# Performance work log

Measured on AMD Instinct MI355X. Metric: run time of the kernel, lower is better.

## Reference

```python
import jax, jax.numpy as jnp
import numpy as np


def _iterative_pinv(mat, n_iter=6):
    # mat: [b, h, m, m]
    m = mat.shape[-1]
    I = jnp.eye(m, dtype=mat.dtype)
    # global (over all batch/heads) scaling, matching torch.max over full tensor
    init_coef = jnp.max(jnp.sum(jnp.abs(mat), axis=-2)) * jnp.max(jnp.sum(jnp.abs(mat), axis=-1))
    out = jnp.swapaxes(mat, -2, -1) / init_coef
    for _ in range(n_iter):
        mo = jnp.matmul(mat, out)          # [b,h,m,m]
        term1 = 7.0 * I - mo
        term2 = 15.0 * I - jnp.matmul(mo, term1)
        term3 = 13.0 * I - jnp.matmul(mo, term2)
        out = 0.25 * jnp.matmul(out, term3)
    return out


def _landmarks(x, m):
    # x: [b, h, s, d] -> segment means [b, h, m, d]
    b, h, s, d = x.shape
    l = s // m
    return x.reshape(b, h, m, l, d).mean(axis=-2)


def setup_inputs() -> dict:
    key = jax.random.key(0)
    kq, kk, kv = jax.random.split(key, 3)
    shape = (4, 12, 4096, 64)
    return {
        "query": jax.random.normal(kq, shape, dtype=jnp.float32),
        "key": jax.random.normal(kk, shape, dtype=jnp.float32),
        "value": jax.random.normal(kv, shape, dtype=jnp.float32),
        "num_landmarks": 64,
    }


def reference(query, key, value, num_landmarks):
    b, h, s, d = query.shape
    scale = 1.0 / jnp.sqrt(jnp.asarray(d, dtype=query.dtype))
    q_lm = _landmarks(query, num_landmarks)   # [b,h,m,d]
    k_lm = _landmarks(key, num_landmarks)     # [b,h,m,d]
    # F_tilde: [b,h,s,m]
    F_tilde = jax.nn.softmax(jnp.einsum('bhsd,bhmd->bhsm', query, k_lm) * scale, axis=-1)
    # A_tilde: pinv of [b,h,m,m]
    A_tilde = _iterative_pinv(
        jax.nn.softmax(jnp.einsum('bhnd,bhmd->bhnm', q_lm, k_lm) * scale, axis=-1))
    # B_tilde: [b,h,m,s]
    B_tilde = jax.nn.softmax(jnp.einsum('bhmd,bhsd->bhms', q_lm, key) * scale, axis=-1)
    # out = F_tilde @ (A_tilde @ (B_tilde @ value))  -> [b,h,s,d]
    bv = jnp.matmul(B_tilde, value)        # [b,h,m,d]
    abv = jnp.matmul(A_tilde, bv)          # [b,h,m,d]
    return jnp.matmul(F_tilde, abv)        # [b,h,s,d]
```

## Files before the change

### kernel.cpp

```cpp
#include <hip/hip_runtime.h>
#include <math.h>

#define BH 48
#define Ss 4096
#define Dd 64
#define Mm 64
#define NCH 16
#define SCALE 0.125f
#define PLN 4096

typedef unsigned int u32;
typedef unsigned short u16;
typedef __attribute__((ext_vector_type(8))) short short8;
typedef __attribute__((ext_vector_type(4))) float floatx4;

union FRAG { uint4 u; short8 s; };

#define MFMA(a,b,c) __builtin_amdgcn_mfma_f32_16x16x32_bf16(a,b,c,0,0,0)

__device__ __forceinline__ u32 pack2_hi(float a, float b) {
    return (__float_as_uint(a) >> 16) | (__float_as_uint(b) & 0xFFFF0000u);
}
__device__ __forceinline__ float trunc_bf(float a) {
    return __uint_as_float(__float_as_uint(a) & 0xFFFF0000u);
}
__device__ __forceinline__ void split1(float v, u16& h, u16& l) {
    u32 u = __float_as_uint(v);
    h = (u16)(u >> 16);
    float r = v - __uint_as_float(u & 0xFFFF0000u);
    l = (u16)(__float_as_uint(r) >> 16);
}
__device__ __forceinline__ void split8(const float* v, short8& h, short8& l) {
    FRAG H, L;
    float r[8];
#pragma unroll
    for (int i = 0; i < 8; i++) r[i] = v[i] - trunc_bf(v[i]);
    H.u.x = pack2_hi(v[0], v[1]); H.u.y = pack2_hi(v[2], v[3]);
    H.u.z = pack2_hi(v[4], v[5]); H.u.w = pack2_hi(v[6], v[7]);
    L.u.x = pack2_hi(r[0], r[1]); L.u.y = pack2_hi(r[2], r[3]);
    L.u.z = pack2_hi(r[4], r[5]); L.u.w = pack2_hi(r[6], r[7]);
    h = H.s; l = L.s;
}
__device__ __forceinline__ int swz(int row, int col) {
    return row * 64 + ((((col >> 3) ^ (row & 7)) << 3) | (col & 7));
}

__global__ __launch_bounds__(256) void k_landmarks(const float* __restrict__ Q,
                                                   const float* __restrict__ Kg,
                                                   float* __restrict__ qlm,
                                                   float* __restrict__ klm,
                                                   u16* __restrict__ qlmh, u16* __restrict__ qlml,
                                                   u16* __restrict__ klmh, u16* __restrict__ klml) {
    int g = blockIdx.x, bh = blockIdx.y;
    int t = threadIdx.x;
    int seg = t >> 4, d4 = t & 15;
    int m = g * 16 + seg;
    const float* src = blockIdx.z ? Kg : Q;
    float* dst = blockIdx.z ? klm : qlm;
    u16* dh = blockIdx.z ? klmh : qlmh;
    u16* dl = blockIdx.z ? klml : qlml;
    const float* base = src + ((size_t)bh * Ss + (size_t)m * 64) * Dd + d4 * 4;
    float4 acc = make_float4(0.f, 0.f, 0.f, 0.f);
#pragma unroll
    for (int l = 0; l < 64; l++) {
        float4 v = *(const float4*)(base + (size_t)l * Dd);
        acc.x += v.x; acc.y += v.y; acc.z += v.z; acc.w += v.w;
    }
    acc.x *= (1.f / 64.f); acc.y *= (1.f / 64.f);
    acc.z *= (1.f / 64.f); acc.w *= (1.f / 64.f);
    int idx = (bh * Mm + m) * Dd + d4 * 4;
    *(float4*)(dst + idx) = acc;
    float vv[4] = {acc.x, acc.y, acc.z, acc.w};
    u16 hh[4], ll[4];
#pragma unroll
    for (int i = 0; i < 4; i++) split1(vv[i], hh[i], ll[i]);
    *(uint2*)(dh + idx) = make_uint2((u32)hh[0] | ((u32)hh[1] << 16), (u32)hh[2] | ((u32)hh[3] << 16));
    *(uint2*)(dl + idx) = make_uint2((u32)ll[0] | ((u32)ll[1] << 16), (u32)ll[2] | ((u32)ll[3] << 16));
}

__global__ __launch_bounds__(256) void k_lmsm(const float* __restrict__ qlm,
                                              const float* __restrict__ klm,
                                              float* __restrict__ smat,
                                              unsigned int* __restrict__ coef) {
    int bh = blockIdx.x, t = threadIdx.x;
    __shared__ float kl[Mm * Dd];
    __shared__ float ql[Mm * Dd];
    __shared__ float Lp[Mm][Mm + 1];
    const float4* kb = (const float4*)(klm + bh * Mm * Dd);
    const float4* qb = (const float4*)(qlm + bh * Mm * Dd);
    for (int i = t; i < Mm * Dd / 4; i += 256) {
        ((float4*)kl)[i] = kb[i];
        ((float4*)ql)[i] = qb[i];
    }
    __syncthreads();
    int n = t >> 2, c = t & 3;
    float p[16];
#pragma unroll
    for (int jj = 0; jj < 16; jj++) {
        int m = c * 16 + jj;
        float s = 0.f;
#pragma unroll
        for (int d4 = 0; d4 < 16; d4++) {
            int d = (((d4 + c * 4) & 15)) * 4;
            float4 kv = *(const float4*)(kl + m * Dd + d);
            float4 qv = *(const float4*)(ql + n * Dd + d);
            s += qv.x * kv.x + qv.y * kv.y + qv.z * kv.z + qv.w * kv.w;
        }
        p[jj] = s * SCALE;
    }
    float mx = -INFINITY;
#pragma unroll
    for (int jj = 0; jj < 16; jj++) mx = fmaxf(mx, p[jj]);
    mx = fmaxf(mx, __shfl_xor(mx, 1));
    mx = fmaxf(mx, __shfl_xor(mx, 2));
    float den = 0.f;
#pragma unroll
    for (int jj = 0; jj < 16; jj++) { p[jj] = __expf(p[jj] - mx); den += p[jj]; }
    den += __shfl_xor(den, 1);
    den += __shfl_xor(den, 2);
    float inv = 1.0f / den;
#pragma unroll
    for (int jj = 0; jj < 16; jj++) Lp[n][c * 16 + jj] = p[jj] * inv;
    __syncthreads();
    float* sg = smat + bh * Mm * Mm;
    for (int i = t; i < Mm * Mm; i += 256) sg[i] = Lp[i >> 6][i & 63];
    if (t < Mm) {
        float cs = 0.f;
#pragma unroll
        for (int nn = 0; nn < Mm; nn++) cs += Lp[nn][t];
#pragma unroll
        for (int off = 1; off < 64; off <<= 1) cs = fmaxf(cs, __shfl_xor(cs, off));
        if (t == 0) atomicMax(coef + 0, __float_as_uint(cs));
    } else if (t < 2 * Mm) {
        int nn = t - Mm; float rs = 0.f;
#pragma unroll
        for (int m = 0; m < Mm; m++) rs += Lp[nn][m];
#pragma unroll
        for (int off = 1; off < 64; off <<= 1) rs = fmaxf(rs, __shfl_xor(rs, off));
        if (t == Mm) atomicMax(coef + 1, __float_as_uint(rs));
    }
}

__device__ __forceinline__ void pinv_pass(const u16* __restrict__ Ah, const u16* __restrict__ Al,
                                          const u16* __restrict__ Bph, const u16* __restrict__ Bpl,
                                          u16* __restrict__ Oh, u16* __restrict__ Ol,
                                          int w, int c, int hi,
                                          float diag, float sgn, float scl) {
    short8 bfh[2], bfl[2];
#pragma unroll
    for (int ks = 0; ks < 2; ks++) {
        bfh[ks] = *(const short8*)&Bph[swz(w * 16 + c, ks * 32 + hi * 8)];
        bfl[ks] = *(const short8*)&Bpl[swz(w * 16 + c, ks * 32 + hi * 8)];
    }
    int j = w * 16 + c;
#pragma unroll
    for (int ta = 0; ta < 4; ta++) {
        floatx4 acc = (floatx4){0.f, 0.f, 0.f, 0.f};
#pragma unroll
        for (int ks = 0; ks < 2; ks++) {
            short8 afh = *(const short8*)&Ah[swz(ta * 16 + c, ks * 32 + hi * 8)];
            short8 afl = *(const short8*)&Al[swz(ta * 16 + c, ks * 32 + hi * 8)];
            acc = MFMA(afh, bfh[ks], acc);
            acc = MFMA(afl, bfh[ks], acc);
            acc = MFMA(afh, bfl[ks], acc);
        }
        u16 oh[4], ol[4];
#pragma unroll
        for (int r = 0; r < 4; r++) {
            int i = ta * 16 + hi * 4 + r;
            float v = scl * (((i == j) ? diag : 0.f) + sgn * acc[r]);
            split1(v, oh[r], ol[r]);
        }
        int o0 = swz(j, ta * 16 + hi * 4);
        *(u32*)&Oh[o0]     = (u32)oh[0] | ((u32)oh[1] << 16);
        *(u32*)&Oh[o0 + 2] = (u32)oh[2] | ((u32)oh[3] << 16);
        *(u32*)&Ol[o0]     = (u32)ol[0] | ((u32)ol[1] << 16);
        *(u32*)&Ol[o0 + 2] = (u32)ol[2] | ((u32)ol[3] << 16);
    }
}

__global__ __launch_bounds__(256) void k_pinv(const float* __restrict__ smat,
                                              const unsigned int* __restrict__ coef,
                                              float* __restrict__ atil) {
    extern __shared__ u16 P[];
    u16* FaH  = P;             u16* FaL  = P + PLN;
    u16* FxcH = P + 2 * PLN;   u16* FxcL = P + 3 * PLN;
    u16* X0H  = P + 4 * PLN;   u16* X0L  = P + 5 * PLN;
    u16* X1H  = P + 6 * PLN;   u16* X1L  = P + 7 * PLN;
    u16* T1H  = P + 8 * PLN;   u16* T1L  = P + 9 * PLN;
    u16* T2H  = P + 10 * PLN;  u16* T2L  = P + 11 * PLN;
    int bh = blockIdx.x, t = threadIdx.x;
    int w = t >> 6, l = t & 63, c = l & 15, hi = l >> 4;
    float inv = 1.0f / (__uint_as_float(coef[0]) * __uint_as_float(coef[1]));
    {
        int r = t >> 2, kq = (t & 3) * 16;
        const float* ar = smat + bh * 4096 + r * 64 + kq;
        float v[16];
#pragma unroll
        for (int q = 0; q < 4; q++) {
            float4 x = *(const float4*)(ar + q * 4);
            v[q * 4 + 0] = x.x; v[q * 4 + 1] = x.y; v[q * 4 + 2] = x.z; v[q * 4 + 3] = x.w;
        }
        short8 h0, l0, h1, l1;
        split8(v, h0, l0); split8(v + 8, h1, l1);
        *(short8*)&FaH[swz(r, kq)] = h0;     *(short8*)&FaH[swz(r, kq + 8)] = h1;
        *(short8*)&FaL[swz(r, kq)] = l0;     *(short8*)&FaL[swz(r, kq + 8)] = l1;
        float vs[16];
#pragma unroll
        for (int q = 0; q < 16; q++) vs[q] = v[q] * inv;
        split8(vs, h0, l0); split8(vs + 8, h1, l1);
        *(short8*)&FxcH[swz(r, kq)] = h0;    *(short8*)&FxcH[swz(r, kq + 8)] = h1;
        *(short8*)&FxcL[swz(r, kq)] = l0;    *(short8*)&FxcL[swz(r, kq + 8)] = l1;
#pragma unroll
        for (int q = 0; q < 16; q++) {
            u16 h, lo; split1(vs[q], h, lo);
            X0H[swz(kq + q, r)] = h;
            X0L[swz(kq + q, r)] = lo;
        }
    }
    __syncthreads();
    u16 *xrH = X0H, *xrL = X0L, *moH = X1H, *moL = X1L;
    for (int it = 0; it < 6; it++) {
        pinv_pass(FxcH, FxcL, FaH, FaL, moH, moL, w, c, hi, 0.f, 1.f, 1.f);
        pinv_pass(FaH, FaL, FxcH, FxcL, T1H, T1L, w, c, hi, 7.f, -1.f, 1.f);
        __syncthreads();
        pinv_pass(moH, moL, T1H, T1L, T2H, T2L, w, c, hi, 15.f, -1.f, 1.f);
        __syncthreads();
        pinv_pass(moH, moL, T2H, T2L, T1H, T1L, w, c, hi, 13.f, -1.f, 1.f);
        __syncthreads();
        pinv_pass(T1H, T1L, xrH, xrL, moH, moL, w, c, hi, 0.f, 1.f, 0.25f);
        pinv_pass(xrH, xrL, T1H, T1L, FxcH, FxcL, w, c, hi, 0.f, 1.f, 0.25f);
        __syncthreads();
        u16* th = xrH; xrH = moH; moH = th;
        u16* tl = xrL; xrL = moL; moL = tl;
    }
    {
        int i = t >> 2, j0 = (t & 3) * 16;
        FRAG h0, l0, h1, l1;
        h0.s = *(const short8*)&xrH[swz(i, j0)];
        l0.s = *(const short8*)&xrL[swz(i, j0)];
        h1.s = *(const short8*)&xrH[swz(i, j0 + 8)];
        l1.s = *(const short8*)&xrL[swz(i, j0 + 8)];
        float* ob = atil + bh * 4096 + i * 64 + j0;
#pragma unroll
        for (int q = 0; q < 8; q++) {
            ob[q]     = __uint_as_float(((u32)(u16)h0.s[q]) << 16) + __uint_as_float(((u32)(u16)l0.s[q]) << 16);
            ob[q + 8] = __uint_as_float(((u32)(u16)h1.s[q]) << 16) + __uint_as_float(((u32)(u16)l1.s[q]) << 16);
        }
    }
}

__global__ __launch_bounds__(256) void k_bvp(const float* __restrict__ Kg,
                                             const float* __restrict__ Vg,
                                             const u16* __restrict__ qlmh,
                                             const u16* __restrict__ qlml,
                                             float* __restrict__ pnum,
                                             float* __restrict__ pden) {
    __shared__ __align__(16) u16 Pb[2][4096];
    __shared__ __align__(16) u16 vt[2][4096];
    __shared__ __align__(16) float tmp[64 * 68];
    int ch = blockIdx.x, bh = blockIdx.y;
    int t = threadIdx.x, w = t >> 6, l = t & 63, c = l & 15, hi = l >> 4;
    const float* Kbh = Kg + (size_t)bh * Ss * Dd;
    const float* Vbh = Vg + (size_t)bh * Ss * Dd;
    const u16* qh = qlmh + bh * Mm * Dd;
    const u16* ql = qlml + bh * Mm * Dd;
    floatx4 pvC[4];
    float denacc[16];
#pragma unroll
    for (int i = 0; i < 4; i++) pvC[i] = (floatx4){0.f, 0.f, 0.f, 0.f};
#pragma unroll
    for (int i = 0; i < 16; i++) denacc[i] = 0.f;

    for (int tile = 0; tile < 4; ++tile) {
        int s0 = ch * 256 + tile * 64;
        __syncthreads();
        {
            int sl = t >> 2, q = (t & 3) * 16;
            const float4* vp = (const float4*)(Vbh + (size_t)(s0 + sl) * Dd + q);
            float4* dp = (float4*)(tmp + sl * 68 + q);
#pragma unroll
            for (int qq = 0; qq < 4; qq++) dp[qq] = vp[qq];
        }
        {
            int srow = s0 + w * 16 + c;
            const float* kp = Kbh + (size_t)srow * Dd + hi * 8;
            short8 kbh[2], kbl[2];
#pragma unroll
            for (int ks = 0; ks < 2; ks++) {
                float kv[8];
                float4 a = *(const float4*)(kp + ks * 32);
                float4 b = *(const float4*)(kp + ks * 32 + 4);
                kv[0] = a.x; kv[1] = a.y; kv[2] = a.z; kv[3] = a.w;
                kv[4] = b.x; kv[5] = b.y; kv[6] = b.z; kv[7] = b.w;
                split8(kv, kbh[ks], kbl[ks]);
            }
            floatx4 qkC[4];
#pragma unroll
            for (int i = 0; i < 4; i++) qkC[i] = (floatx4){0.f, 0.f, 0.f, 0.f};
#pragma unroll
            for (int mt = 0; mt < 4; mt++) {
#pragma unroll
                for (int ks = 0; ks < 2; ks++) {
                    short8 aH = *(const short8*)&qh[(mt * 16 + c) * 64 + ks * 32 + hi * 8];
                    short8 aL = *(const short8*)&ql[(mt * 16 + c) * 64 + ks * 32 + hi * 8];
                    qkC[mt] = MFMA(aH, kbh[ks], qkC[mt]);
                    qkC[mt] = MFMA(aL, kbh[ks], qkC[mt]);
                    qkC[mt] = MFMA(aH, kbl[ks], qkC[mt]);
                }
            }
#pragma unroll
            for (int mt = 0; mt < 4; mt++) {
#pragma unroll
                for (int r = 0; r < 4; r++) {
                    float pv = __expf(qkC[mt][r] * SCALE);
                    denacc[mt * 4 + r] += pv;
                    int m = mt * 16 + hi * 4 + r;
                    u16 h, lo; split1(pv, h, lo);
                    Pb[0][swz(m, w * 16 + c)] = h;
                    Pb[1][swz(m, w * 16 + c)] = lo;
                }
            }
        }
        __syncthreads();
        {
            int d = t >> 2, sg = t & 3;
            float v[16];
#pragma unroll
            for (int j = 0; j < 16; j++) v[j] = tmp[(sg * 16 + j) * 68 + d];
            short8 h0, l0, h1, l1;
            split8(v, h0, l0); split8(v + 8, h1, l1);
            *(short8*)&vt[0][swz(d, sg * 16)] = h0;
            *(short8*)&vt[0][swz(d, sg * 16 + 8)] = h1;
            *(short8*)&vt[1][swz(d, sg * 16)] = l0;
            *(short8*)&vt[1][swz(d, sg * 16 + 8)] = l1;
        }
        __syncthreads();
#pragma unroll
        for (int ks = 0; ks < 2; ks++) {
            short8 pah = *(const short8*)&Pb[0][swz(w * 16 + c, ks * 32 + hi * 8)];
            short8 pal = *(const short8*)&Pb[1][swz(w * 16 + c, ks * 32 + hi * 8)];
#pragma unroll
            for (int dt = 0; dt < 4; dt++) {
                short8 vh = *(const short8*)&vt[0][swz(dt * 16 + c, ks * 32 + hi * 8)];
                short8 vl = *(const short8*)&vt[1][swz(dt * 16 + c, ks * 32 + hi * 8)];
                pvC[dt] = MFMA(pah, vh, pvC[dt]);
                pvC[dt] = MFMA(pal, vh, pvC[dt]);
                pvC[dt] = MFMA(pah, vl, pvC[dt]);
            }
        }
    }
    float* nb = pnum + (size_t)(bh * NCH + ch) * 4096;
#pragma unroll
    for (int dt = 0; dt < 4; dt++)
#pragma unroll
        for (int r = 0; r < 4; r++)
            nb[(w * 16 + hi * 4 + r) * 64 + dt * 16 + c] = pvC[dt][r];
#pragma unroll
    for (int i = 0; i < 16; i++) {
        float v = denacc[i];
        v += __shfl_xor(v, 1); v += __shfl_xor(v, 2);
        v += __shfl_xor(v, 4); v += __shfl_xor(v, 8);
        denacc[i] = v;
    }
    if (c == 0) {
        float* db = pden + (size_t)((bh * NCH + ch) * 4 + w) * 64;
#pragma unroll
        for (int mt = 0; mt < 4; mt++)
#pragma unroll
            for (int r = 0; r < 4; r++)
                db[mt * 16 + hi * 4 + r] = denacc[mt * 4 + r];
    }
}

__global__ __launch_bounds__(256) void k_bvc(const float* __restrict__ pnum,
                                             const float* __restrict__ pden,
                                             const float* __restrict__ atil,
                                             u16* __restrict__ abvh,
                                             u16* __restrict__ abvl) {
    int bh = blockIdx.x, t = threadIdx.x;
    __shared__ float bvs[Mm][Dd + 1];
    __shared__ float Ams[Mm * (Mm + 1)];
    const float* ab = atil + bh * Mm * Mm;
    for (int i = t; i < Mm * Mm; i += 256) Ams[(i >> 6) * 65 + (i & 63)] = ab[i];
    int m = t >> 2, c = t & 3, d0 = c * 16;
    float den = 0.f;
    const float* db = pden + (size_t)bh * NCH * 4 * 64;
#pragma unroll
    for (int i = 0; i < NCH * 4; i++) den += db[i * 64 + m];
    float acc[16];
#pragma unroll
    for (int i = 0; i < 16; i++) acc[i] = 0.f;
    const float* nb = pnum + (size_t)bh * NCH * 4096;
    for (int ch = 0; ch < NCH; ch++) {
        const float4* pa = (const float4*)(nb + ch * 4096 + m * 64 + d0);
#pragma unroll
        for (int q = 0; q < 4; q++) {
            float4 v = pa[q];
            acc[q * 4 + 0] += v.x; acc[q * 4 + 1] += v.y;
            acc[q * 4 + 2] += v.z; acc[q * 4 + 3] += v.w;
        }
    }
    float inv = 1.0f / den;
#pragma unroll
    for (int ii = 0; ii < 16; ii++) bvs[m][d0 + ii] = acc[ii] * inv;
    __syncthreads();
    int j = t & 63, i0 = (t >> 6) << 4;
    float outv[16];
#pragma unroll
    for (int ii = 0; ii < 16; ii++) outv[ii] = 0.f;
#pragma unroll
    for (int k = 0; k < Mm; k++) {
        float bk = bvs[k][j];
#pragma unroll
        for (int ii = 0; ii < 16; ii++) outv[ii] += Ams[(i0 + ii) * 65 + k] * bk;
    }
    u16* oh = abvh + bh * 4096;
    u16* ol = abvl + bh * 4096;
#pragma unroll
    for (int ii = 0; ii < 16; ii++) {
        u16 h, lo; split1(outv[ii], h, lo);
        oh[j * 64 + i0 + ii] = h;
        ol[j * 64 + i0 + ii] = lo;
    }
}

__global__ __launch_bounds__(256) void k_fout(const float* __restrict__ Qg,
                                              const u16* __restrict__ klmh,
                                              const u16* __restrict__ klml,
                                              const u16* __restrict__ abvh,
                                              const u16* __restrict__ abvl,
                                              float* __restrict__ Og) {
    __shared__ __align__(16) u16 skh[4096], skl[4096], sah[4096], sal[4096];
    __shared__ __align__(16) u16 Pw[4][2][1024];
    int sb = blockIdx.x, bh = blockIdx.y;
    int t = threadIdx.x, w = t >> 6, l = t & 63, c = l & 15, hi = l >> 4;
    {
        const uint4* s1 = (const uint4*)(klmh + bh * 4096);
        const uint4* s2 = (const uint4*)(klml + bh * 4096);
        const uint4* s3 = (const uint4*)(abvh + bh * 4096);
        const uint4* s4 = (const uint4*)(abvl + bh * 4096);
#pragma unroll
        for (int i0 = 0; i0 < 512; i0 += 256) {
            int i = i0 + t;
            int row = i >> 3, chk = i & 7;
            int d = row * 8 + (chk ^ (row & 7));
            ((uint4*)skh)[d] = s1[i];
            ((uint4*)skl)[d] = s2[i];
            ((uint4*)sah)[d] = s3[i];
            ((uint4*)sal)[d] = s4[i];
        }
    }
    const float* qbase = Qg + ((size_t)bh * Ss + (size_t)sb * 256 + w * 16 + c) * Dd + hi * 8;
    float4 qv0[4];
    qv0[0] = *(const float4*)(qbase + 0);
    qv0[1] = *(const float4*)(qbase + 4);
    qv0[2] = *(const float4*)(qbase + 32);
    qv0[3] = *(const float4*)(qbase + 36);
    __syncthreads();
#pragma unroll
    for (int ti = 0; ti < 4; ti++) {
        float4 qn[4];
        if (ti < 3) {
            const float* q2 = qbase + (ti + 1) * 64 * Dd;
            qn[0] = *(const float4*)(q2 + 0);
            qn[1] = *(const float4*)(q2 + 4);
            qn[2] = *(const float4*)(q2 + 32);
            qn[3] = *(const float4*)(q2 + 36);
        }
        short8 qah[2], qal[2];
        {
            float qq[8];
            qq[0] = qv0[0].x; qq[1] = qv0[0].y; qq[2] = qv0[0].z; qq[3] = qv0[0].w;
            qq[4] = qv0[1].x; qq[5] = qv0[1].y; qq[6] = qv0[1].z; qq[7] = qv0[1].w;
            split8(qq, qah[0], qal[0]);
            qq[0] = qv0[2].x; qq[1] = qv0[2].y; qq[2] = qv0[2].z; qq[3] = qv0[2].w;
            qq[4] = qv0[3].x; qq[5] = qv0[3].y; qq[6] = qv0[3].z; qq[7] = qv0[3].w;
            split8(qq, qah[1], qal[1]);
        }
        floatx4 qkC[4];
#pragma unroll
        for (int i = 0; i < 4; i++) qkC[i] = (floatx4){0.f, 0.f, 0.f, 0.f};
        __builtin_amdgcn_s_setprio(1);
#pragma unroll
        for (int mt = 0; mt < 4; mt++) {
#pragma unroll
            for (int ks = 0; ks < 2; ks++) {
                short8 bH = *(const short8*)&skh[swz(mt * 16 + c, ks * 32 + hi * 8)];
                short8 bL = *(const short8*)&skl[swz(mt * 16 + c, ks * 32 + hi * 8)];
                qkC[mt] = MFMA(qah[ks], bH, qkC[mt]);
                qkC[mt] = MFMA(qal[ks], bH, qkC[mt]);
                qkC[mt] = MFMA(qah[ks], bL, qkC[mt]);
            }
        }
        __builtin_amdgcn_s_setprio(0);
        float p[16], dsum[4];
#pragma unroll
        for (int r = 0; r < 4; r++) dsum[r] = 0.f;
#pragma unroll
        for (int mt = 0; mt < 4; mt++)
#pragma unroll
            for (int r = 0; r < 4; r++) {
                float pv = __expf(qkC[mt][r] * SCALE);
                p[mt * 4 + r] = pv;
                dsum[r] += pv;
            }
#pragma unroll
        for (int r = 0; r < 4; r++) {
            float v = dsum[r];
            v += __shfl_xor(v, 1); v += __shfl_xor(v, 2);
            v += __shfl_xor(v, 4); v += __shfl_xor(v, 8);
            dsum[r] = 1.0f / v;
        }
#pragma unroll
        for (int mt = 0; mt < 4; mt++)
#pragma unroll
            for (int r = 0; r < 4; r++) {
                float pv = p[mt * 4 + r] * dsum[r];
                u16 h, lo; split1(pv, h, lo);
                Pw[w][0][swz(hi * 4 + r, mt * 16 + c)] = h;
                Pw[w][1][swz(hi * 4 + r, mt * 16 + c)] = lo;
            }
        asm volatile("s_waitcnt lgkmcnt(0)" ::: "memory");
        __builtin_amdgcn_sched_barrier(0);
        short8 pah[2], pal[2];
#pragma unroll
        for (int ks = 0; ks < 2; ks++) {
            pah[ks] = *(const short8*)&Pw[w][0][swz(c, ks * 32 + hi * 8)];
            pal[ks] = *(const short8*)&Pw[w][1][swz(c, ks * 32 + hi * 8)];
        }
        floatx4 oC[4];
#pragma unroll
        for (int i = 0; i < 4; i++) oC[i] = (floatx4){0.f, 0.f, 0.f, 0.f};
        __builtin_amdgcn_s_setprio(1);
#pragma unroll
        for (int dt = 0; dt < 4; dt++) {
#pragma unroll
            for (int ks = 0; ks < 2; ks++) {
                short8 bH = *(const short8*)&sah[swz(dt * 16 + c, ks * 32 + hi * 8)];
                short8 bL = *(const short8*)&sal[swz(dt * 16 + c, ks * 32 + hi * 8)];
                oC[dt] = MFMA(pah[ks], bH, oC[dt]);
                oC[dt] = MFMA(pal[ks], bH, oC[dt]);
                oC[dt] = MFMA(pah[ks], bL, oC[dt]);
            }
        }
        __builtin_amdgcn_s_setprio(0);
        float* ob = Og + ((size_t)bh * Ss + (size_t)sb * 256 + ti * 64 + w * 16) * Dd;
#pragma unroll
        for (int dt = 0; dt < 4; dt++)
#pragma unroll
            for (int r = 0; r < 4; r++)
                ob[(hi * 4 + r) * 64 + dt * 16 + c] = oC[dt][r];
        qv0[0] = qn[0]; qv0[1] = qn[1]; qv0[2] = qn[2]; qv0[3] = qn[3];
    }
}

extern "C" void kernel_launch(void* const* d_in, const int* in_sizes, int n_in,
                              void* d_out, int out_size, void* d_ws, size_t ws_size,
                              hipStream_t stream) {
    const float* Q = (const float*)d_in[0];
    const float* K = (const float*)d_in[1];
    const float* V = (const float*)d_in[2];
    float* out = (float*)d_out;
    float* ws = (float*)d_ws;
    unsigned int* coef = (unsigned int*)d_ws;
    float* qlm  = ws + 16;
    float* klm  = qlm  + BH * Mm * Dd;
    float* smat = klm  + BH * Mm * Dd;
    float* atil = smat + BH * Mm * Mm;
    float* pnum = atil + BH * Mm * Mm;
    float* pden = pnum + (size_t)BH * NCH * Mm * Dd;
    u16* ub   = (u16*)(pden + (size_t)BH * NCH * 4 * 64);
    u16* qlmh = ub;
    u16* qlml = qlmh + BH * Mm * Dd;
    u16* klmh = qlml + BH * Mm * Dd;
    u16* klml = klmh + BH * Mm * Dd;
    u16* abvh = klml + BH * Mm * Dd;
    u16* abvl = abvh + BH * Mm * Dd;

    hipMemsetAsync(d_ws, 0, 64, stream);

    k_landmarks<<<dim3(4, BH, 2), dim3(256), 0, stream>>>(Q, K, qlm, klm, qlmh, qlml, klmh, klml);
    k_lmsm<<<dim3(BH), dim3(256), 0, stream>>>(qlm, klm, smat, coef);
    k_pinv<<<dim3(BH), dim3(256), 12 * PLN * 2, stream>>>(smat, coef, atil);
    k_bvp<<<dim3(NCH, BH), dim3(256), 0, stream>>>(K, V, qlmh, qlml, pnum, pden);
    k_bvc<<<dim3(BH), dim3(256), 0, stream>>>(pnum, pden, atil, abvh, abvl);
    k_fout<<<dim3(Ss / 256, BH), dim3(256), 0, stream>>>(Q, klmh, klml, abvh, abvl, out);
}
```

Baseline: 148.9 us.

## Prefetch next K/V tile into registers and stage q landmarks in LDS

The k_bvp kernel now loads the next tile's K and V rows into registers while the current tile is computed, double-buffering global loads across the four-tile loop. The q-landmark hi/lo bf16 fragments are copied once into swizzled shared memory instead of being re-read from global memory per MFMA. MFMA sections are wrapped in s_setprio, and the transposed V read order is rotated to reduce LDS bank conflicts. The cost is more registers and extra LDS, which could lower occupancy.

```diff
diff --git a/kernel.cpp b/kernel.cpp
--- a/kernel.cpp
+++ b/kernel.cpp
@@ -256,6 +256,7 @@
                                              const u16* __restrict__ qlml,
                                              float* __restrict__ pnum,
                                              float* __restrict__ pden) {
+    __shared__ __align__(16) u16 qsh[4096], qsl[4096];
     __shared__ __align__(16) u16 Pb[2][4096];
     __shared__ __align__(16) u16 vt[2][4096];
     __shared__ __align__(16) float tmp[64 * 68];
@@ -263,71 +264,100 @@
     int t = threadIdx.x, w = t >> 6, l = t & 63, c = l & 15, hi = l >> 4;
     const float* Kbh = Kg + (size_t)bh * Ss * Dd;
     const float* Vbh = Vg + (size_t)bh * Ss * Dd;
-    const u16* qh = qlmh + bh * Mm * Dd;
-    const u16* ql = qlml + bh * Mm * Dd;
+    {
+        const uint4* s1 = (const uint4*)(qlmh + bh * 4096);
+        const uint4* s2 = (const uint4*)(qlml + bh * 4096);
+#pragma unroll
+        for (int i0 = 0; i0 < 512; i0 += 256) {
+            int i = i0 + t;
+            int row = i >> 3, chk = i & 7;
+            int d = row * 8 + (chk ^ (row & 7));
+            ((uint4*)qsh)[d] = s1[i];
+            ((uint4*)qsl)[d] = s2[i];
+        }
+    }
     floatx4 pvC[4];
     float denacc[16];
 #pragma unroll
     for (int i = 0; i < 4; i++) pvC[i] = (floatx4){0.f, 0.f, 0.f, 0.f};
 #pragma unroll
     for (int i = 0; i < 16; i++) denacc[i] = 0.f;
-
+    int sl = t >> 2, qoff = (t & 3) * 16;
+    const float* kp0 = Kbh + (size_t)(ch * 256 + w * 16 + c) * Dd + hi * 8;
+    const float* vp0 = Vbh + (size_t)(ch * 256 + sl) * Dd + qoff;
+    float4 kv[2][4], vv[2][4];
+    kv[0][0] = *(const float4*)(kp0 + 0);
+    kv[0][1] = *(const float4*)(kp0 + 4);
+    kv[0][2] = *(const float4*)(kp0 + 32);
+    kv[0][3] = *(const float4*)(kp0 + 36);
+#pragma unroll
+    for (int q = 0; q < 4; q++) vv[0][q] = *(const float4*)(vp0 + q * 4);
+    __syncthreads();
+#pragma unroll
     for (int tile = 0; tile < 4; ++tile) {
-        int s0 = ch * 256 + tile * 64;
-        __syncthreads();
+        const int cur = tile & 1, nxt = cur ^ 1;
+        if (tile < 3) {
+            const float* kp = kp0 + (size_t)(tile + 1) * 64 * Dd;
+            const float* vp = vp0 + (size_t)(tile + 1) * 64 * Dd;
+            kv[nxt][0] = *(const float4*)(kp + 0);
+            kv[nxt][1] = *(const float4*)(kp + 4);
+            kv[nxt][2] = *(const float4*)(kp + 32);
+            kv[nxt][3] = *(const float4*)(kp + 36);
+#pragma unroll
+            for (int q = 0; q < 4; q++) vv[nxt][q] = *(const float4*)(vp + q * 4);
+        }
+        short8 kbh[2], kbl[2];
         {
-            int sl = t >> 2, q = (t & 3) * 16;
-            const float4* vp = (const float4*)(Vbh + (size_t)(s0 + sl) * Dd + q);
-            float4* dp = (float4*)(tmp + sl * 68 + q);
-#pragma unroll
-            for (int qq = 0; qq < 4; qq++) dp[qq] = vp[qq];
+            float kq[8];
+            kq[0] = kv[cur][0].x; kq[1] = kv[cur][0].y; kq[2] = kv[cur][0].z; kq[3] = kv[cur][0].w;
+            kq[4] = kv[cur][1].x; kq[5] = kv[cur][1].y; kq[6] = kv[cur][1].z; kq[7] = kv[cur][1].w;
+            split8(kq, kbh[0], kbl[0]);
+            kq[0] = kv[cur][2].x; kq[1] = kv[cur][2].y; kq[2] = kv[cur][2].z; kq[3] = kv[cur][2].w;
+            kq[4] = kv[cur][3].x; kq[5] = kv[cur][3].y; kq[6] = kv[cur][3].z; kq[7] = kv[cur][3].w;
+            split8(kq, kbh[1], kbl[1]);
+        }
+        floatx4 qkC[4];
+#pragma unroll
+        for (int i = 0; i < 4; i++) qkC[i] = (floatx4){0.f, 0.f, 0.f, 0.f};
+        __builtin_amdgcn_s_setprio(1);
+#pragma unroll
+        for (int mt = 0; mt < 4; mt++) {
+#pragma unroll
+            for (int ks = 0; ks < 2; ks++) {
+                short8 aH = *(const short8*)&qsh[swz(mt * 16 + c, ks * 32 + hi * 8)];
+                short8 aL = *(const short8*)&qsl[swz(mt * 16 + c, ks * 32 + hi * 8)];
+                qkC[mt] = MFMA(aH, kbh[ks], qkC[mt]);
+                qkC[mt] = MFMA(aL, kbh[ks], qkC[mt]);
+                qkC[mt] = MFMA(aH, kbl[ks], qkC[mt]);
+            }
+        }
+        __builtin_amdgcn_s_setprio(0);
+#pragma unroll
+        for (int mt = 0; mt < 4; mt++) {
+#pragma unroll
+            for (int r = 0; r < 4; r++) {
+                float pv = __expf(qkC[mt][r] * SCALE);
+                denacc[mt * 4 + r] += pv;
+                int m = mt * 16 + hi * 4 + r;
+                u16 h, lo; split1(pv, h, lo);
+                Pb[0][swz(m, w * 16 + c)] = h;
+                Pb[1][swz(m, w * 16 + c)] = lo;
+            }
         }
         {
-            int srow = s0 + w * 16 + c;
-            const float* kp = Kbh + (size_t)srow * Dd + hi * 8;
-            short8 kbh[2], kbl[2];
-#pragma unroll
-            for (int ks = 0; ks < 2; ks++) {
-                float kv[8];
-                float4 a = *(const float4*)(kp + ks * 32);
-                float4 b = *(const float4*)(kp + ks * 32 + 4);
-                kv[0] = a.x; kv[1] = a.y; kv[2] = a.z; kv[3] = a.w;
-                kv[4] = b.x; kv[5] = b.y; kv[6] = b.z; kv[7] = b.w;
-                split8(kv, kbh[ks], kbl[ks]);
-            }
-            floatx4 qkC[4];
-#pragma unroll
-            for (int i = 0; i < 4; i++) qkC[i] = (floatx4){0.f, 0.f, 0.f, 0.f};
-#pragma unroll
-            for (int mt = 0; mt < 4; mt++) {
-#pragma unroll
-                for (int ks = 0; ks < 2; ks++) {
-                    short8 aH = *(const short8*)&qh[(mt * 16 + c) * 64 + ks * 32 + hi * 8];
-                    short8 aL = *(const short8*)&ql[(mt * 16 + c) * 64 + ks * 32 + hi * 8];
-                    qkC[mt] = MFMA(aH, kbh[ks], qkC[mt]);
-                    qkC[mt] = MFMA(aL, kbh[ks], qkC[mt]);
-                    qkC[mt] = MFMA(aH, kbl[ks], qkC[mt]);
-                }
-            }
-#pragma unroll
-            for (int mt = 0; mt < 4; mt++) {
-#pragma unroll
-                for (int r = 0; r < 4; r++) {
-                    float pv = __expf(qkC[mt][r] * SCALE);
-                    denacc[mt * 4 + r] += pv;
-                    int m = mt * 16 + hi * 4 + r;
-                    u16 h, lo; split1(pv, h, lo);
-                    Pb[0][swz(m, w * 16 + c)] = h;
-                    Pb[1][swz(m, w * 16 + c)] = lo;
-                }
-            }
+            float4* dp = (float4*)(tmp + sl * 68 + qoff);
+            dp[0] = vv[cur][0]; dp[1] = vv[cur][1];
+            dp[2] = vv[cur][2]; dp[3] = vv[cur][3];
         }
         __syncthreads();
         {
             int d = t >> 2, sg = t & 3;
             float v[16];
 #pragma unroll
-            for (int j = 0; j < 16; j++) v[j] = tmp[(sg * 16 + j) * 68 + d];
+            for (int jj = 0; jj < 16; jj++) {
+                int j = (jj + sg * 4) & 15;
+                v[j] = tmp[(sg * 16 + j) * 68 + d];
+            }
             short8 h0, l0, h1, l1;
             split8(v, h0, l0); split8(v + 8, h1, l1);
             *(short8*)&vt[0][swz(d, sg * 16)] = h0;
@@ -336,6 +366,7 @@
             *(short8*)&vt[1][swz(d, sg * 16 + 8)] = l1;
         }
         __syncthreads();
+        __builtin_amdgcn_s_setprio(1);
 #pragma unroll
         for (int ks = 0; ks < 2; ks++) {
             short8 pah = *(const short8*)&Pb[0][swz(w * 16 + c, ks * 32 + hi * 8)];
@@ -349,6 +380,8 @@
                 pvC[dt] = MFMA(pah, vl, pvC[dt]);
             }
         }
+        __builtin_amdgcn_s_setprio(0);
+        __syncthreads();
     }
     float* nb = pnum + (size_t)(bh * NCH + ch) * 4096;
 #pragma unroll
```

Measured after the change: 169.8 us. 14.1% more time.
